# Kernel optimization log

Hardware: AMD Instinct MI355X
Metric: run time of the kernel (lower is better)

## Reference

```python
import math
import jax, jax.numpy as jnp
import numpy as np

B, T, D, H = 2, 2048, 1024, 16
N_LAYERS = 24


def get_slopes(n):
    def pow2(n):
        start = 2 ** (-2 ** (-(math.log2(n) - 3)))
        return [start * start ** i for i in range(n)]
    if math.log2(n).is_integer():
        return pow2(n)
    c = 2 ** math.floor(math.log2(n))
    return pow2(c) + get_slopes(2 * c)[0::2][: n - c]


def setup_inputs() -> dict:
    key = jax.random.key(0)
    ks = jax.random.split(key, 5)
    x = jax.random.normal(ks[0], (B, T, D), dtype=jnp.float32)
    Wq = 0.02 * jax.random.normal(ks[1], (D, D), dtype=jnp.float32)
    Wk = 0.02 * jax.random.normal(ks[2], (D, D), dtype=jnp.float32)
    Wv = 0.02 * jax.random.normal(ks[3], (D, D), dtype=jnp.float32)
    Wo = (0.02 / math.sqrt(2 * N_LAYERS)) * jax.random.normal(ks[4], (D, D), dtype=jnp.float32)
    z = jnp.zeros((D,), dtype=jnp.float32)
    return {"x": x, "Wq": Wq, "bq": z, "Wk": Wk, "bk": z, "Wv": Wv, "bv": z, "Wo": Wo, "bo": z}


def reference(x, Wq, bq, Wk, bk, Wv, bv, Wo, bo):
    Bb, Tt, C = x.shape
    hd = C // H
    # QKV projections -> (B, H, T, hd)
    q = (x @ Wq + bq).reshape(Bb, Tt, H, hd).transpose(0, 2, 1, 3)
    k = (x @ Wk + bk).reshape(Bb, Tt, H, hd).transpose(0, 2, 1, 3)
    v = (x @ Wv + bv).reshape(Bb, Tt, H, hd).transpose(0, 2, 1, 3)
    # scaled dot-product scores (B, H, T, T)
    attn = jnp.einsum('bhqd,bhkd->bhqk', q, k) / jnp.sqrt(jnp.asarray(hd, x.dtype))
    # ALiBi bias: module uses only last row of the relative-position matrix,
    # broadcast over query positions: -slope_h * (T-1 - j), shape (1, H, 1, T)
    slopes = jnp.asarray(get_slopes(H), dtype=x.dtype)
    alibi = -slopes[None, :, None, None] * (Tt - 1 - jnp.arange(Tt, dtype=x.dtype))[None, None, None, :]
    attn = attn + alibi
    # causal mask
    causal = jnp.tril(jnp.ones((Tt, Tt), dtype=bool))[None, None, :, :]
    attn = jnp.where(causal, attn, jnp.finfo(x.dtype).min)
    p = jax.nn.softmax(attn, axis=-1)
    out = jnp.einsum('bhqk,bhkd->bqhd', p, v).reshape(Bb, Tt, C)
    return out @ Wo + bo
```

## Files before the change

kernel.cpp:

```cpp
#include <hip/hip_runtime.h>
#include <hip/hip_bf16.h>

#define Bn 2
#define Tdim 2048
#define Ddim 1024
#define Hn 16
#define HD 64

typedef unsigned short u16;
typedef unsigned int u32;
typedef __attribute__((ext_vector_type(8))) __bf16 bf16x8;
typedef __attribute__((ext_vector_type(4))) float f32x4;
typedef __attribute__((ext_vector_type(16))) float f32x16;
typedef __attribute__((ext_vector_type(4))) u32 u32x4;

struct alignas(8) U16x4 { u16 x, y, z, w; };

__device__ __forceinline__ u16 f2bf(float f) {
  union { float f; u32 i; } v; v.f = f;
  u32 x = v.i;
  u32 r = (x + 0x7fffu + ((x >> 16) & 1u)) >> 16;
  return (u16)r;
}
__device__ __forceinline__ u32 pk2bf(float a, float b) {
  return (u32)f2bf(a) | ((u32)f2bf(b) << 16);
}

__device__ __forceinline__ void cp16(const u16* g, u16* l) {
  __builtin_amdgcn_global_load_lds(
      (const __attribute__((address_space(1))) u32*)g,
      (__attribute__((address_space(3))) u32*)l, 16, 0, 0);
}

__device__ __forceinline__ f32x4 mfma16(bf16x8 a, bf16x8 b, f32x4 c) {
  return __builtin_amdgcn_mfma_f32_16x16x32_bf16(a, b, c, 0, 0, 0);
}
__device__ __forceinline__ f32x16 mfma32(bf16x8 a, bf16x8 b, f32x16 c) {
  return __builtin_amdgcn_mfma_f32_32x32x16_bf16(a, b, c, 0, 0, 0);
}

__global__ __launch_bounds__(256) void convert_x(const float* __restrict__ src,
                                                 u16* __restrict__ dst) {
  const int i = (blockIdx.x * 256 + threadIdx.x) * 8;
  u16 t[8];
#pragma unroll
  for (int j = 0; j < 8; j++) t[j] = f2bf(src[i + j]);
  *(bf16x8*)&dst[i] = *(const bf16x8*)t;
}

__global__ __launch_bounds__(256) void transpose_k(
    const float* __restrict__ s0, const float* __restrict__ s1,
    const float* __restrict__ s2, const float* __restrict__ s3,
    u16* __restrict__ dst) {
  const float* src = (blockIdx.z == 0) ? s0 : (blockIdx.z == 1) ? s1
                   : (blockIdx.z == 2) ? s2 : s3;
  u16* d = dst + (size_t)blockIdx.z * Ddim * Ddim;
  __shared__ u16 tile[32][33];
  const int tx = threadIdx.x, ty = threadIdx.y;
  const int x = blockIdx.x * 32 + tx;
  const int y0 = blockIdx.y * 32;
#pragma unroll
  for (int j = 0; j < 32; j += 8) tile[ty + j][tx] = f2bf(src[(size_t)(y0 + ty + j) * Ddim + x]);
  __syncthreads();
  const int xo = blockIdx.y * 32 + tx;
  const int yo0 = blockIdx.x * 32;
#pragma unroll
  for (int j = 0; j < 32; j += 8) d[(size_t)(yo0 + ty + j) * Ddim + xo] = tile[tx][ty + j];
}

__global__ __launch_bounds__(256, 2) void gemm_qkv(
    const u16* __restrict__ Xb, const u16* __restrict__ WT,
    const float* __restrict__ bq, const float* __restrict__ bk, const float* __restrict__ bv,
    u16* __restrict__ Q, u16* __restrict__ K, u16* __restrict__ Vt) {
  const int z = blockIdx.z;
  const u16* Wt = WT + (size_t)z * Ddim * Ddim;
  const float* bias = (z == 0) ? bq : (z == 1) ? bk : bv;
  u16* QK = (z == 0) ? Q : K;

  __shared__ alignas(16) u16 Alds[128 * 32];
  __shared__ alignas(16) u16 Blds[128 * 32];
  const int tid = threadIdx.x;
  const int w = tid >> 6, lane = tid & 63, ln = lane & 15, quad = lane >> 4;
  const int wm = (w >> 1) * 64, wn = (w & 1) * 64;
  const int tm = blockIdx.x * 128, tn = blockIdx.y * 128;

  f32x4 acc[4][4] = {};

  const int srow = tid >> 2, scol = (tid & 3) * 8;
  const u16* ag = Xb + (size_t)(tm + srow) * Ddim + scol;
  const u16* ag2 = ag + (size_t)64 * Ddim;
  const u16* bg = Wt + (size_t)(tn + srow) * Ddim + scol;
  const u16* bg2 = bg + (size_t)64 * Ddim;
  u16* al = &Alds[w * 512];
  u16* al2 = &Alds[2048 + w * 512];
  u16* bl = &Blds[w * 512];
  u16* bl2 = &Blds[2048 + w * 512];

  for (int k0 = 0; k0 < Ddim; k0 += 32) {
    __syncthreads();
    cp16(ag + k0, al);
    cp16(ag2 + k0, al2);
    cp16(bg + k0, bl);
    cp16(bg2 + k0, bl2);
    __syncthreads();
    bf16x8 af[4], bfr[4];
#pragma unroll
    for (int i = 0; i < 4; i++)
      af[i] = *(const bf16x8*)&Alds[(wm + i * 16 + ln) * 32 + quad * 8];
#pragma unroll
    for (int i = 0; i < 4; i++)
      bfr[i] = *(const bf16x8*)&Blds[(wn + i * 16 + ln) * 32 + quad * 8];
#pragma unroll
    for (int mi = 0; mi < 4; mi++)
#pragma unroll
      for (int ni = 0; ni < 4; ni++)
        acc[mi][ni] = mfma16(af[mi], bfr[ni], acc[mi][ni]);
  }

#pragma unroll
  for (int mi = 0; mi < 4; mi++) {
#pragma unroll
    for (int ni = 0; ni < 4; ni++) {
      const int gm0 = tm + wm + mi * 16 + quad * 4;
      const int gn = tn + wn + ni * 16 + ln;
      const float bv_ = bias[gn];
      const int hh = gn >> 6, dd = gn & 63;
      const int b0 = gm0 >> 11, t0 = gm0 & 2047;
      if (z < 2) {
        u16* p = QK + (((size_t)(b0 * Hn + hh) * Tdim) + t0) * HD + dd;
#pragma unroll
        for (int r = 0; r < 4; r++) p[r * HD] = f2bf(acc[mi][ni][r] + bv_);
      } else {
        U16x4 pk;
        pk.x = f2bf(acc[mi][ni][0] + bv_);
        pk.y = f2bf(acc[mi][ni][1] + bv_);
        pk.z = f2bf(acc[mi][ni][2] + bv_);
        pk.w = f2bf(acc[mi][ni][3] + bv_);
        *(U16x4*)&Vt[((size_t)(b0 * Hn + hh) * HD + dd) * Tdim + t0] = pk;
      }
    }
  }
}

#define KSTR 68
#define VSTR 132
__global__ __launch_bounds__(256, 2) void attn_k(
    const u16* __restrict__ Q, const u16* __restrict__ K, const u16* __restrict__ Vt,
    u16* __restrict__ O) {
  __shared__ alignas(16) u16 Klds[128 * KSTR];
  __shared__ alignas(16) u16 Vtlds[64 * VSTR];

  const int qb = (int)gridDim.x - 1 - (int)blockIdx.x;
  const int bh = blockIdx.y;
  const int b = bh >> 4, hh = bh & 15;
  const int q0 = qb * 128;
  const int tid = threadIdx.x;
  const int w = tid >> 6, lane = tid & 63;
  const int qi = lane & 31, hf = lane >> 5;

  const u16* Qh = Q + (size_t)bh * Tdim * HD;
  const u16* Kh = K + (size_t)bh * Tdim * HD;
  const u16* Vh = Vt + (size_t)bh * HD * Tdim;
  const float slope = exp2f(-0.5f * (float)(hh + 1));

  const int tg = q0 + w * 32 + qi;
  const float tterm = slope * (float)tg + 3.0f;

  bf16x8 qf[4];
#pragma unroll
  for (int kc = 0; kc < 4; kc++)
    qf[kc] = *(const bf16x8*)&Qh[(size_t)tg * HD + kc * 16 + hf * 8];

  float lsum = 0.f;
  f32x16 oacc[2] = {};
  const int nkt = qb + 1;

  bf16x8 kreg[4], vreg[4];
#pragma unroll
  for (int c = 0; c < 4; c++) {
    const int e = c * 2048 + tid * 8;
    kreg[c] = *(const bf16x8*)&Kh[(size_t)(e >> 6) * HD + (e & 63)];
    vreg[c] = *(const bf16x8*)&Vh[(size_t)(e >> 7) * Tdim + (e & 127)];
  }

  for (int kt = 0; kt < nkt; kt++) {
    const int kb = kt * 128;
    __syncthreads();
#pragma unroll
    for (int c = 0; c < 4; c++) {
      const int e = c * 2048 + tid * 8;
      *(bf16x8*)&Klds[(e >> 6) * KSTR + (e & 63)] = kreg[c];
      *(bf16x8*)&Vtlds[(e >> 7) * VSTR + (e & 127)] = vreg[c];
    }
    __syncthreads();

    if (kt + 1 < nkt) {
      const int kb2 = kb + 128;
#pragma unroll
      for (int c = 0; c < 4; c++) {
        const int e = c * 2048 + tid * 8;
        kreg[c] = *(const bf16x8*)&Kh[(size_t)(kb2 + (e >> 6)) * HD + (e & 63)];
        vreg[c] = *(const bf16x8*)&Vh[(size_t)(e >> 7) * Tdim + kb2 + (e & 127)];
      }
    }

    f32x16 st[4] = {};
#pragma unroll
    for (int kc = 0; kc < 4; kc++) {
#pragma unroll
      for (int ni = 0; ni < 4; ni++) {
        bf16x8 kf = *(const bf16x8*)&Klds[(ni * 32 + qi) * KSTR + kc * 16 + hf * 8];
        st[ni] = mfma32(kf, qf[kc], st[ni]);
      }
    }

    const bool diag = (kt == nkt - 1);
    bf16x8 pfrag[8];
#pragma unroll
    for (int ni = 0; ni < 4; ni++) {
      float p[16];
#pragma unroll
      for (int ri = 0; ri < 16; ri++) {
        const int n = kb + ni * 32 + (ri & 3) + 8 * (ri >> 2) + 4 * hf;
        float pv = __expf(st[ni][ri] * 0.125f + slope * (float)n - tterm);
        if (diag && n > tg) pv = 0.f;
        lsum += pv;
        p[ri] = pv;
      }
      u32 pk[4][2];
#pragma unroll
      for (int g = 0; g < 4; g++) {
        pk[g][0] = pk2bf(p[g * 4 + 0], p[g * 4 + 1]);
        pk[g][1] = pk2bf(p[g * 4 + 2], p[g * 4 + 3]);
      }
#pragma unroll
      for (int a = 0; a < 2; a++) {
        const u32 own0 = (hf == 0) ? pk[2 * a][0] : pk[2 * a + 1][0];
        const u32 own1 = (hf == 0) ? pk[2 * a][1] : pk[2 * a + 1][1];
        const u32 snd0 = (hf == 0) ? pk[2 * a + 1][0] : pk[2 * a][0];
        const u32 snd1 = (hf == 0) ? pk[2 * a + 1][1] : pk[2 * a][1];
        const u32 rcv0 = (u32)__shfl_xor((int)snd0, 32);
        const u32 rcv1 = (u32)__shfl_xor((int)snd1, 32);
        u32x4 fr;
        fr.x = (hf == 0) ? own0 : rcv0;
        fr.y = (hf == 0) ? own1 : rcv1;
        fr.z = (hf == 0) ? rcv0 : own0;
        fr.w = (hf == 0) ? rcv1 : own1;
        pfrag[ni * 2 + a] = *(bf16x8*)&fr;
      }
    }

#pragma unroll
    for (int kf16 = 0; kf16 < 8; kf16++) {
#pragma unroll
      for (int nd = 0; nd < 2; nd++) {
        bf16x8 vf = *(const bf16x8*)&Vtlds[(nd * 32 + qi) * VSTR + kf16 * 16 + hf * 8];
        oacc[nd] = mfma32(pfrag[kf16], vf, oacc[nd]);
      }
    }
  }

  lsum += __shfl_xor(lsum, 32);

  float rinv[16];
#pragma unroll
  for (int ri = 0; ri < 16; ri++) {
    const int rq = (ri & 3) + 8 * (ri >> 2) + 4 * hf;
    rinv[ri] = 1.0f / __shfl(lsum, rq);
  }
#pragma unroll
  for (int nd = 0; nd < 2; nd++) {
#pragma unroll
    for (int ri = 0; ri < 16; ri++) {
      const int rq = (ri & 3) + 8 * (ri >> 2) + 4 * hf;
      const int t = q0 + w * 32 + rq;
      O[((size_t)(b * Tdim + t)) * Ddim + hh * HD + nd * 32 + qi] =
          f2bf(oacc[nd][ri] * rinv[ri]);
    }
  }
}

__global__ __launch_bounds__(256, 2) void gemm_out(
    const u16* __restrict__ A, const u16* __restrict__ WoT, const float* __restrict__ bo,
    float* __restrict__ C) {
  __shared__ alignas(16) u16 Alds[128 * 32];
  __shared__ alignas(16) u16 Blds[128 * 32];
  const int tid = threadIdx.x;
  const int w = tid >> 6, lane = tid & 63, ln = lane & 15, quad = lane >> 4;
  const int wm = (w >> 1) * 64, wn = (w & 1) * 64;
  const int tm = blockIdx.x * 128, tn = blockIdx.y * 128;

  f32x4 acc[4][4] = {};

  const int srow = tid >> 2, scol = (tid & 3) * 8;
  const u16* ag = A + (size_t)(tm + srow) * Ddim + scol;
  const u16* ag2 = ag + (size_t)64 * Ddim;
  const u16* bg = WoT + (size_t)(tn + srow) * Ddim + scol;
  const u16* bg2 = bg + (size_t)64 * Ddim;
  u16* al = &Alds[w * 512];
  u16* al2 = &Alds[2048 + w * 512];
  u16* bl = &Blds[w * 512];
  u16* bl2 = &Blds[2048 + w * 512];

  for (int k0 = 0; k0 < Ddim; k0 += 32) {
    __syncthreads();
    cp16(ag + k0, al);
    cp16(ag2 + k0, al2);
    cp16(bg + k0, bl);
    cp16(bg2 + k0, bl2);
    __syncthreads();
    bf16x8 af[4], bfr[4];
#pragma unroll
    for (int i = 0; i < 4; i++)
      af[i] = *(const bf16x8*)&Alds[(wm + i * 16 + ln) * 32 + quad * 8];
#pragma unroll
    for (int i = 0; i < 4; i++)
      bfr[i] = *(const bf16x8*)&Blds[(wn + i * 16 + ln) * 32 + quad * 8];
#pragma unroll
    for (int mi = 0; mi < 4; mi++)
#pragma unroll
      for (int ni = 0; ni < 4; ni++)
        acc[mi][ni] = mfma16(af[mi], bfr[ni], acc[mi][ni]);
  }

#pragma unroll
  for (int mi = 0; mi < 4; mi++) {
#pragma unroll
    for (int ni = 0; ni < 4; ni++) {
      const int gm0 = tm + wm + mi * 16 + quad * 4;
      const int gn = tn + wn + ni * 16 + ln;
      const float bv_ = bo[gn];
#pragma unroll
      for (int r = 0; r < 4; r++)
        C[(size_t)(gm0 + r) * Ddim + gn] = acc[mi][ni][r] + bv_;
    }
  }
}

extern "C" void kernel_launch(void* const* d_in, const int* in_sizes, int n_in,
                              void* d_out, int out_size, void* d_ws, size_t ws_size,
                              hipStream_t stream) {
  (void)in_sizes; (void)n_in; (void)out_size; (void)ws_size;
  const float* x  = (const float*)d_in[0];
  const float* Wq = (const float*)d_in[1];
  const float* bq = (const float*)d_in[2];
  const float* Wk = (const float*)d_in[3];
  const float* bk = (const float*)d_in[4];
  const float* Wv = (const float*)d_in[5];
  const float* bv = (const float*)d_in[6];
  const float* Wo = (const float*)d_in[7];
  const float* bo = (const float*)d_in[8];

  char* ws = (char*)d_ws;
  const size_t MB = 1024 * 1024;
  u16* WT  = (u16*)(ws + 0 * MB);
  u16* Qb  = (u16*)(ws + 8 * MB);
  u16* Kb  = (u16*)(ws + 16 * MB);
  u16* Vtb = (u16*)(ws + 24 * MB);
  u16* Xb  = (u16*)(ws + 32 * MB);
  u16* AO  = (u16*)(ws + 32 * MB);
  u16* WoT = WT + (size_t)3 * Ddim * Ddim;

  convert_x<<<dim3(2048), 256, 0, stream>>>(x, Xb);
  transpose_k<<<dim3(32, 32, 4), dim3(32, 8), 0, stream>>>(Wq, Wk, Wv, Wo, WT);

  gemm_qkv<<<dim3(32, 8, 3), 256, 0, stream>>>(Xb, WT, bq, bk, bv, Qb, Kb, Vtb);
  attn_k<<<dim3(16, 32), 256, 0, stream>>>(Qb, Kb, Vtb, AO);
  gemm_out<<<dim3(32, 8), 256, 0, stream>>>(AO, WoT, bo, (float*)d_out);
}
```

Before: 219.2 us.

## Split attention KV range across two blocks and merge partials

```diff
diff --git a/kernel.cpp b/kernel.cpp
--- a/kernel.cpp
+++ b/kernel.cpp
@@ -22,8 +22,11 @@
   u32 r = (x + 0x7fffu + ((x >> 16) & 1u)) >> 16;
   return (u16)r;
 }
-__device__ __forceinline__ u32 pk2bf(float a, float b) {
-  return (u32)f2bf(a) | ((u32)f2bf(b) << 16);
+__device__ __forceinline__ float bf2f(u16 u) {
+  union { u32 i; float f; } v; v.i = ((u32)u) << 16; return v.f;
+}
+__device__ __forceinline__ u32 fbits(float f) {
+  union { float f; u32 i; } v; v.f = f; return v.i;
 }
 
 __device__ __forceinline__ void cp16(const u16* g, u16* l) {
@@ -144,15 +147,17 @@
 
 #define KSTR 68
 #define VSTR 132
+#define L2E 1.44269504088896f
 __global__ __launch_bounds__(256, 2) void attn_k(
     const u16* __restrict__ Q, const u16* __restrict__ K, const u16* __restrict__ Vt,
-    u16* __restrict__ O) {
+    u16* __restrict__ Op, float* __restrict__ lp) {
   __shared__ alignas(16) u16 Klds[128 * KSTR];
   __shared__ alignas(16) u16 Vtlds[64 * VSTR];
 
-  const int qb = (int)gridDim.x - 1 - (int)blockIdx.x;
+  const int bx = blockIdx.x;
+  const int qb = 15 - (bx >> 1);
+  const int s = bx & 1;
   const int bh = blockIdx.y;
-  const int b = bh >> 4, hh = bh & 15;
   const int q0 = qb * 128;
   const int tid = threadIdx.x;
   const int w = tid >> 6, lane = tid & 63;
@@ -161,10 +166,23 @@
   const u16* Qh = Q + (size_t)bh * Tdim * HD;
   const u16* Kh = K + (size_t)bh * Tdim * HD;
   const u16* Vh = Vt + (size_t)bh * HD * Tdim;
-  const float slope = exp2f(-0.5f * (float)(hh + 1));
+  const float slope = exp2f(-0.5f * (float)((bh & 15) + 1));
+
+  const int nkt = qb + 1;
+  const int h0 = (nkt + 1) >> 1;
+  const int kt0 = s ? h0 : 0;
+  const int kt1 = s ? nkt : h0;
 
   const int tg = q0 + w * 32 + qi;
-  const float tterm = slope * (float)tg + 3.0f;
+  const float sl2 = slope * L2E;
+  const float c1 = 0.125f * L2E;
+  const float tt2 = (slope * (float)tg + 3.0f) * L2E;
+  const float f4hf = (float)(4 * hf);
+  float sg8[4], slm[4];
+#pragma unroll
+  for (int g = 0; g < 4; g++) sg8[g] = sl2 * (float)(8 * g);
+#pragma unroll
+  for (int m = 0; m < 4; m++) slm[m] = sl2 * (float)m;
 
   bf16x8 qf[4];
 #pragma unroll
@@ -173,17 +191,19 @@
 
   float lsum = 0.f;
   f32x16 oacc[2] = {};
-  const int nkt = qb + 1;
 
   bf16x8 kreg[4], vreg[4];
-#pragma unroll
-  for (int c = 0; c < 4; c++) {
-    const int e = c * 2048 + tid * 8;
-    kreg[c] = *(const bf16x8*)&Kh[(size_t)(e >> 6) * HD + (e & 63)];
-    vreg[c] = *(const bf16x8*)&Vh[(size_t)(e >> 7) * Tdim + (e & 127)];
-  }
-
-  for (int kt = 0; kt < nkt; kt++) {
+  {
+    const int kb = kt0 * 128;
+#pragma unroll
+    for (int c = 0; c < 4; c++) {
+      const int e = c * 2048 + tid * 8;
+      kreg[c] = *(const bf16x8*)&Kh[(size_t)(kb + (e >> 6)) * HD + (e & 63)];
+      vreg[c] = *(const bf16x8*)&Vh[(size_t)(e >> 7) * Tdim + kb + (e & 127)];
+    }
+  }
+
+  for (int kt = kt0; kt < kt1; kt++) {
     const int kb = kt * 128;
     __syncthreads();
 #pragma unroll
@@ -194,7 +214,7 @@
     }
     __syncthreads();
 
-    if (kt + 1 < nkt) {
+    if (kt + 1 < kt1) {
       const int kb2 = kb + 128;
 #pragma unroll
       for (int c = 0; c < 4; c++) {
@@ -215,37 +235,48 @@
     }
 
     const bool diag = (kt == nkt - 1);
+    const float fkb = (float)kb + f4hf;
     bf16x8 pfrag[8];
 #pragma unroll
     for (int ni = 0; ni < 4; ni++) {
-      float p[16];
-#pragma unroll
-      for (int ri = 0; ri < 16; ri++) {
-        const int n = kb + ni * 32 + (ri & 3) + 8 * (ri >> 2) + 4 * hf;
-        float pv = __expf(st[ni][ri] * 0.125f + slope * (float)n - tterm);
-        if (diag && n > tg) pv = 0.f;
-        lsum += pv;
-        p[ri] = pv;
+      const float cni = __builtin_fmaf(sl2, fkb + (float)(32 * ni), -tt2);
+      u32 pu[16];
+      if (!diag) {
+#pragma unroll
+        for (int ri = 0; ri < 16; ri++) {
+          const float e = __builtin_fmaf(st[ni][ri], c1, cni + sg8[ri >> 2] + slm[ri & 3]);
+          const float p = __builtin_amdgcn_exp2f(e);
+          lsum += p;
+          pu[ri] = fbits(p) + 0x8000u;
+        }
+      } else {
+#pragma unroll
+        for (int ri = 0; ri < 16; ri++) {
+          const int n = kb + ni * 32 + (ri & 3) + 8 * (ri >> 2) + 4 * hf;
+          const float e = __builtin_fmaf(st[ni][ri], c1, cni + sg8[ri >> 2] + slm[ri & 3]);
+          float p = __builtin_amdgcn_exp2f(e);
+          if (n > tg) p = 0.f;
+          lsum += p;
+          pu[ri] = fbits(p) + 0x8000u;
+        }
       }
       u32 pk[4][2];
 #pragma unroll
       for (int g = 0; g < 4; g++) {
-        pk[g][0] = pk2bf(p[g * 4 + 0], p[g * 4 + 1]);
-        pk[g][1] = pk2bf(p[g * 4 + 2], p[g * 4 + 3]);
+        pk[g][0] = __builtin_amdgcn_perm(pu[g * 4 + 1], pu[g * 4 + 0], 0x07060302u);
+        pk[g][1] = __builtin_amdgcn_perm(pu[g * 4 + 3], pu[g * 4 + 2], 0x07060302u);
       }
 #pragma unroll
       for (int a = 0; a < 2; a++) {
-        const u32 own0 = (hf == 0) ? pk[2 * a][0] : pk[2 * a + 1][0];
-        const u32 own1 = (hf == 0) ? pk[2 * a][1] : pk[2 * a + 1][1];
         const u32 snd0 = (hf == 0) ? pk[2 * a + 1][0] : pk[2 * a][0];
         const u32 snd1 = (hf == 0) ? pk[2 * a + 1][1] : pk[2 * a][1];
         const u32 rcv0 = (u32)__shfl_xor((int)snd0, 32);
         const u32 rcv1 = (u32)__shfl_xor((int)snd1, 32);
         u32x4 fr;
-        fr.x = (hf == 0) ? own0 : rcv0;
-        fr.y = (hf == 0) ? own1 : rcv1;
-        fr.z = (hf == 0) ? rcv0 : own0;
-        fr.w = (hf == 0) ? rcv1 : own1;
+        fr.x = (hf == 0) ? pk[2 * a][0] : rcv0;
+        fr.y = (hf == 0) ? pk[2 * a][1] : rcv1;
+        fr.z = (hf == 0) ? rcv0 : pk[2 * a + 1][0];
+        fr.w = (hf == 0) ? rcv1 : pk[2 * a + 1][1];
         pfrag[ni * 2 + a] = *(bf16x8*)&fr;
       }
     }
@@ -261,23 +292,38 @@
   }
 
   lsum += __shfl_xor(lsum, 32);
-
-  float rinv[16];
-#pragma unroll
-  for (int ri = 0; ri < 16; ri++) {
-    const int rq = (ri & 3) + 8 * (ri >> 2) + 4 * hf;
-    rinv[ri] = 1.0f / __shfl(lsum, rq);
-  }
+  if (hf == 0) lp[(size_t)s * 65536 + bh * Tdim + tg] = lsum;
+
+  u16* Ob = Op + (size_t)s * (32u * Tdim * HD) + ((size_t)bh * Tdim) * HD;
 #pragma unroll
   for (int nd = 0; nd < 2; nd++) {
 #pragma unroll
     for (int ri = 0; ri < 16; ri++) {
       const int rq = (ri & 3) + 8 * (ri >> 2) + 4 * hf;
       const int t = q0 + w * 32 + rq;
-      O[((size_t)(b * Tdim + t)) * Ddim + hh * HD + nd * 32 + qi] =
-          f2bf(oacc[nd][ri] * rinv[ri]);
-    }
-  }
+      Ob[(size_t)t * HD + nd * 32 + qi] = f2bf(oacc[nd][ri]);
+    }
+  }
+}
+
+__global__ __launch_bounds__(256) void merge_k(const u16* __restrict__ Op,
+                                               const float* __restrict__ lp,
+                                               u16* __restrict__ AO) {
+  const int i = blockIdx.x * 256 + threadIdx.x;
+  const int d8 = i & 7;
+  const int t = (i >> 3) & 2047;
+  const int bh = i >> 14;
+  const int b = bh >> 4, h = bh & 15;
+  const float l = lp[bh * Tdim + t] + lp[65536 + bh * Tdim + t];
+  const float inv = 1.0f / l;
+  const size_t off = ((size_t)bh * Tdim + t) * HD + d8 * 8;
+  const u16* O0 = Op + off;
+  const u16* O1 = Op + (size_t)32 * Tdim * HD + off;
+  u16 outv[8];
+#pragma unroll
+  for (int j = 0; j < 8; j++)
+    outv[j] = f2bf((bf2f(O0[j]) + bf2f(O1[j])) * inv);
+  *(bf16x8*)&AO[((size_t)(b * Tdim + t)) * Ddim + h * HD + d8 * 8] = *(const bf16x8*)outv;
 }
 
 __global__ __launch_bounds__(256, 2) void gemm_out(
@@ -353,18 +399,21 @@
 
   char* ws = (char*)d_ws;
   const size_t MB = 1024 * 1024;
-  u16* WT  = (u16*)(ws + 0 * MB);
-  u16* Qb  = (u16*)(ws + 8 * MB);
-  u16* Kb  = (u16*)(ws + 16 * MB);
-  u16* Vtb = (u16*)(ws + 24 * MB);
-  u16* Xb  = (u16*)(ws + 32 * MB);
-  u16* AO  = (u16*)(ws + 32 * MB);
+  u16* WT   = (u16*)(ws + 0 * MB);
+  u16* Qb   = (u16*)(ws + 8 * MB);
+  u16* Kb   = (u16*)(ws + 16 * MB);
+  u16* Vtb  = (u16*)(ws + 24 * MB);
+  u16* Xb   = (u16*)(ws + 32 * MB);
+  u16* AO   = (u16*)(ws + 32 * MB);
+  u16* Opart= (u16*)(ws + 40 * MB);
+  float* lpart = (float*)(ws + 56 * MB);
   u16* WoT = WT + (size_t)3 * Ddim * Ddim;
 
   convert_x<<<dim3(2048), 256, 0, stream>>>(x, Xb);
   transpose_k<<<dim3(32, 32, 4), dim3(32, 8), 0, stream>>>(Wq, Wk, Wv, Wo, WT);
 
   gemm_qkv<<<dim3(32, 8, 3), 256, 0, stream>>>(Xb, WT, bq, bk, bv, Qb, Kb, Vtb);
-  attn_k<<<dim3(16, 32), 256, 0, stream>>>(Qb, Kb, Vtb, AO);
+  attn_k<<<dim3(32, 32), 256, 0, stream>>>(Qb, Kb, Vtb, Opart, lpart);
+  merge_k<<<dim3(2048), 256, 0, stream>>>(Opart, lpart, AO);
   gemm_out<<<dim3(32, 8), 256, 0, stream>>>(AO, WoT, bo, (float*)d_out);
 }
```

New measurement: 204.8 us. 6.6% less time.
